# Kernel optimization log

Hardware: AMD Instinct MI355X
Metric: run time of the kernel (lower is better)

Reference implementation:

```python
import jax, jax.numpy as jnp
import numpy as np

CHUNK = 512

def setup_inputs() -> dict:
    key = jax.random.key(0)
    kq, kk, kv = jax.random.split(key, 3)
    shape = (1, 16, 8192, 64)  # B, H, N, E
    return {
        "query": jax.random.normal(kq, shape, dtype=jnp.float32),
        "key": jax.random.normal(kk, shape, dtype=jnp.float32),
        "value": jax.random.normal(kv, shape, dtype=jnp.float32),
    }

def reference(query, key, value):
    c = CHUNK
    B, H, N, E = query.shape
    nc = N // c  # number of query chunks (N assumed divisible by c)
    scale = 1.0 / (E ** 0.5)
    neg_inf = jnp.finfo(query.dtype).min

    qc = query.reshape(B, H, nc, c, E)
    kc = key.reshape(B, H, nc, c, E)
    vc = value.reshape(B, H, nc, c, E)

    # ---- chunk 0: window is just keys[0:c], standard causal mask ----
    s0 = jnp.einsum('bhqe,bhse->bhqs', qc[:, :, 0], kc[:, :, 0]) * scale
    mask0 = jnp.triu(jnp.ones((c, c), dtype=bool), k=1)
    a0 = jax.nn.softmax(jnp.where(mask0, neg_inf, s0), axis=-1)  # (B,H,c,c)
    o0 = jnp.einsum('bhqs,bhse->bhqe', a0, vc[:, :, 0])           # (B,H,c,E)

    # ---- chunks 1..nc-1: key window = [previous chunk, current chunk] ----
    kw = jnp.concatenate([kc[:, :, :-1], kc[:, :, 1:]], axis=3)  # (B,H,nc-1,2c,E)
    vw = jnp.concatenate([vc[:, :, :-1], vc[:, :, 1:]], axis=3)
    s = jnp.einsum('bhnqe,bhnse->bhnqs', qc[:, :, 1:], kw) * scale  # (B,H,nc-1,c,2c)
    # faithful to torch.triu(ones(q_len, k_len), diagonal=1): row r keeps cols 0..r
    mask = jnp.triu(jnp.ones((c, 2 * c), dtype=bool), k=1)
    a = jax.nn.softmax(jnp.where(mask, neg_inf, s), axis=-1)        # (B,H,nc-1,c,2c)
    o = jnp.einsum('bhnqs,bhnse->bhnqe', a, vw)                     # (B,H,nc-1,c,E)

    output = jnp.concatenate([o0, o.reshape(B, H, (nc - 1) * c, E)], axis=2)  # (B,H,N,E)
    # weights concatenated along the key axis (torch cat dim=3)
    a_rest = jnp.moveaxis(a, 2, 3).reshape(B, H, c, (nc - 1) * 2 * c)
    weights = jnp.concatenate([a0, a_rest], axis=3)  # (B,H,c, c + (nc-1)*2c)
    return output, weights
```

## Files before the change

kernel.cpp:

```cpp
#include <hip/hip_runtime.h>

typedef __bf16 bf16x8 __attribute__((ext_vector_type(8)));
typedef float  f32x4  __attribute__((ext_vector_type(4)));

#define NH    16
#define SEQ   8192
#define EDIM  64
#define CHK   512
#define WCOLS 15872
#define OUT0  8388608

#define MFMA(a, b, c) __builtin_amdgcn_mfma_f32_16x16x32_bf16((a), (b), (c), 0, 0, 0)

__global__ __launch_bounds__(512) void chunked_attn_kernel(
    const float* __restrict__ Qg, const float* __restrict__ Kg,
    const float* __restrict__ Vg, float* __restrict__ out)
{
    __shared__ __align__(16) __bf16 lds_k[32768];
    __shared__ __align__(16) __bf16 lds_v[32768];
    __shared__ __align__(16) __bf16 lds_p[8][640];

    const int tid  = threadIdx.x;
    const int lane = tid & 63;
    const int wv   = tid >> 6;
    const int l16  = lane & 15;
    const int quad = lane >> 4;

    const int h  = blockIdx.x >> 4;
    const int n  = blockIdx.x & 15;
    const int ns = (n == 0) ? 0 : n - 1;

    const size_t qbase = ((size_t)h * SEQ + (size_t)n  * CHK) * EDIM;
    const size_t kbase = ((size_t)h * SEQ + (size_t)ns * CHK) * EDIM;
    float* __restrict__ W = out + OUT0;
    const size_t wrow0  = (size_t)h * CHK;
    const int    colbase = (n == 0) ? 0 : (CHK + (n - 1) * 2 * CHK);

    if (n != 0) {
        const size_t z0 = wrow0 * WCOLS + (size_t)(colbase + CHK);
        #pragma unroll 4
        for (int idx = tid; idx < 512 * 128; idx += 512) {
            const int r = idx >> 7, j = idx & 127;
            f32x4 z = {0.f, 0.f, 0.f, 0.f};
            *(f32x4*)(W + z0 + (size_t)r * WCOLS + (size_t)(j * 4)) = z;
        }
    }

    #pragma unroll
    for (int it = 0; it < 8; ++it) {
        const int c = tid + it * 512;
        const int s = c >> 3, sub = c & 7;
        const float* src = Kg + kbase + (size_t)s * EDIM + sub * 8;
        const float4 a = *(const float4*)src;
        const float4 b = *(const float4*)(src + 4);
        bf16x8 t;
        t[0] = (__bf16)a.x; t[1] = (__bf16)a.y; t[2] = (__bf16)a.z; t[3] = (__bf16)a.w;
        t[4] = (__bf16)b.x; t[5] = (__bf16)b.y; t[6] = (__bf16)b.z; t[7] = (__bf16)b.w;
        const int idx = ((s >> 4) * 8 + sub) * 16 + (s & 15);
        ((bf16x8*)lds_k)[idx] = t;
    }

    #pragma unroll
    for (int it = 0; it < 8; ++it) {
        const int c = tid + it * 512;
        const int e = c & 63, sb = c >> 6;
        bf16x8 t;
        #pragma unroll
        for (int j = 0; j < 8; ++j)
            t[j] = (__bf16)Vg[kbase + (size_t)(sb * 8 + j) * EDIM + e];
        const int idx = (((sb >> 2) * 4 + (e >> 4)) * 4 + (sb & 3)) * 16 + (e & 15);
        ((bf16x8*)lds_v)[idx] = t;
    }

    __syncthreads();

    const float SC = 0.125f * 1.44269504088896340736f;
    __bf16* const pb = lds_p[wv];
    const bf16x8* const kf = (const bf16x8*)lds_k;
    const bf16x8* const vf = (const bf16x8*)lds_v;

    for (int mt = 0; mt < 4; ++mt) {
        const int m0 = wv * 64 + mt * 16;
        const int rq = m0 + quad * 4;

        bf16x8 aq0, aq1;
        {
            const float* qp = Qg + qbase + (size_t)(m0 + l16) * EDIM + quad * 8;
            float4 a = *(const float4*)(qp);
            float4 b = *(const float4*)(qp + 4);
            aq0[0]=(__bf16)(a.x*SC); aq0[1]=(__bf16)(a.y*SC); aq0[2]=(__bf16)(a.z*SC); aq0[3]=(__bf16)(a.w*SC);
            aq0[4]=(__bf16)(b.x*SC); aq0[5]=(__bf16)(b.y*SC); aq0[6]=(__bf16)(b.z*SC); aq0[7]=(__bf16)(b.w*SC);
            a = *(const float4*)(qp + 32);
            b = *(const float4*)(qp + 36);
            aq1[0]=(__bf16)(a.x*SC); aq1[1]=(__bf16)(a.y*SC); aq1[2]=(__bf16)(a.z*SC); aq1[3]=(__bf16)(a.w*SC);
            aq1[4]=(__bf16)(b.x*SC); aq1[5]=(__bf16)(b.y*SC); aq1[6]=(__bf16)(b.z*SC); aq1[7]=(__bf16)(b.w*SC);
        }

        float mr[4] = {-3.0e38f, -3.0e38f, -3.0e38f, -3.0e38f};
        float lr[4] = {0.f, 0.f, 0.f, 0.f};
        for (int t = 0; t < 32; ++t) {
            const int kb = t * 128 + quad * 16 + l16;
            f32x4 acc = {0.f, 0.f, 0.f, 0.f};
            acc = MFMA(aq0, kf[kb],      acc);
            acc = MFMA(aq1, kf[kb + 64], acc);
            const int col = t * 16 + l16;
            #pragma unroll
            for (int r = 0; r < 4; ++r) {
                const bool  keep = col <= rq + r;
                const float s  = acc[r];
                const float nm = keep ? fmaxf(mr[r], s) : mr[r];
                lr[r] = lr[r] * __builtin_amdgcn_exp2f(mr[r] - nm)
                      + (keep ? __builtin_amdgcn_exp2f(s - nm) : 0.f);
                mr[r] = nm;
            }
        }

        float ri[4];
        #pragma unroll
        for (int r = 0; r < 4; ++r) {
            #pragma unroll
            for (int off = 1; off < 16; off <<= 1) {
                const float mo = __shfl_xor(mr[r], off);
                const float lo = __shfl_xor(lr[r], off);
                const float nm = fmaxf(mr[r], mo);
                lr[r] = lr[r] * __builtin_amdgcn_exp2f(mr[r] - nm)
                      + lo    * __builtin_amdgcn_exp2f(mo    - nm);
                mr[r] = nm;
            }
            ri[r] = __builtin_amdgcn_rcpf(lr[r]);
        }

        f32x4 o0 = {0,0,0,0}, o1 = {0,0,0,0}, o2 = {0,0,0,0}, o3 = {0,0,0,0};
        const size_t wmt = (wrow0 + (size_t)rq) * WCOLS + colbase;
        for (int pr = 0; pr < 16; ++pr) {
            #pragma unroll
            for (int tt = 0; tt < 2; ++tt) {
                const int t  = pr * 2 + tt;
                const int kb = t * 128 + quad * 16 + l16;
                f32x4 acc = {0.f, 0.f, 0.f, 0.f};
                acc = MFMA(aq0, kf[kb],      acc);
                acc = MFMA(aq1, kf[kb + 64], acc);
                const int col = t * 16 + l16;
                #pragma unroll
                for (int r = 0; r < 4; ++r) {
                    const bool  keep = col <= rq + r;
                    const float p = keep
                        ? __builtin_amdgcn_exp2f(acc[r] - mr[r]) * ri[r] : 0.f;
                    W[wmt + (size_t)r * WCOLS + col] = p;
                    pb[(quad * 4 + r) * 40 + tt * 16 + l16] = (__bf16)p;
                }
            }
            const bf16x8 pa = *(const bf16x8*)(pb + l16 * 40 + quad * 8);
            const int vb = pr * 256 + quad * 16 + l16;
            o0 = MFMA(pa, vf[vb      ], o0);
            o1 = MFMA(pa, vf[vb +  64], o1);
            o2 = MFMA(pa, vf[vb + 128], o2);
            o3 = MFMA(pa, vf[vb + 192], o3);
        }

        const size_t ob = qbase + (size_t)rq * EDIM + l16;
        #pragma unroll
        for (int r = 0; r < 4; ++r) {
            out[ob + (size_t)r * EDIM     ] = o0[r];
            out[ob + (size_t)r * EDIM + 16] = o1[r];
            out[ob + (size_t)r * EDIM + 32] = o2[r];
            out[ob + (size_t)r * EDIM + 48] = o3[r];
        }
    }
}

extern "C" void kernel_launch(void* const* d_in, const int* in_sizes, int n_in,
                              void* d_out, int out_size, void* d_ws, size_t ws_size,
                              hipStream_t stream) {
    const float* Q = (const float*)d_in[0];
    const float* K = (const float*)d_in[1];
    const float* V = (const float*)d_in[2];
    float* out = (float*)d_out;
    chunked_attn_kernel<<<dim3(256), dim3(512), 0, stream>>>(Q, K, V, out);
}
```

Baseline: 648.3 us.

## Cache scores in registers, two-pass softmax, vectorized nontemporal weight stores

Stores the 32 score tiles per row group in registers, so QK^T is computed once and the online softmax becomes an exact max pass followed by an exp-sum pass. The weight matrix is written as vectorized 16-byte nontemporal stores of the bf16-rounded probabilities read back from LDS, replacing scalar strided fp32 stores. Zero-fill and output stores are also nontemporal, and launch bounds ask for two blocks per CU. This trades register pressure (128 floats of scores) and weights now rounded to bf16 precision for fewer MFMAs and better coalesced global writes.

```diff
diff --git a/kernel.cpp b/kernel.cpp
--- a/kernel.cpp
+++ b/kernel.cpp
@@ -12,7 +12,7 @@
 
 #define MFMA(a, b, c) __builtin_amdgcn_mfma_f32_16x16x32_bf16((a), (b), (c), 0, 0, 0)
 
-__global__ __launch_bounds__(512) void chunked_attn_kernel(
+__global__ __launch_bounds__(512, 2) void chunked_attn_kernel(
     const float* __restrict__ Qg, const float* __restrict__ Kg,
     const float* __restrict__ Vg, float* __restrict__ out)
 {
@@ -42,7 +42,7 @@
         for (int idx = tid; idx < 512 * 128; idx += 512) {
             const int r = idx >> 7, j = idx & 127;
             f32x4 z = {0.f, 0.f, 0.f, 0.f};
-            *(f32x4*)(W + z0 + (size_t)r * WCOLS + (size_t)(j * 4)) = z;
+            __builtin_nontemporal_store(z, (f32x4*)(W + z0 + (size_t)r * WCOLS + (size_t)(j * 4)));
         }
     }
 
@@ -96,8 +96,8 @@
             aq1[4]=(__bf16)(b.x*SC); aq1[5]=(__bf16)(b.y*SC); aq1[6]=(__bf16)(b.z*SC); aq1[7]=(__bf16)(b.w*SC);
         }
 
-        float mr[4] = {-3.0e38f, -3.0e38f, -3.0e38f, -3.0e38f};
-        float lr[4] = {0.f, 0.f, 0.f, 0.f};
+        f32x4 st[32];
+        #pragma unroll
         for (int t = 0; t < 32; ++t) {
             const int kb = t * 128 + quad * 16 + l16;
             f32x4 acc = {0.f, 0.f, 0.f, 0.f};
@@ -105,52 +105,67 @@
             acc = MFMA(aq1, kf[kb + 64], acc);
             const int col = t * 16 + l16;
             #pragma unroll
+            for (int r = 0; r < 4; ++r)
+                acc[r] = (col <= rq + r) ? acc[r] : -3.0e38f;
+            st[t] = acc;
+        }
+
+        float mr[4];
+        #pragma unroll
+        for (int r = 0; r < 4; ++r) mr[r] = st[0][r];
+        #pragma unroll
+        for (int t = 1; t < 32; ++t) {
+            #pragma unroll
+            for (int r = 0; r < 4; ++r) mr[r] = fmaxf(mr[r], st[t][r]);
+        }
+        #pragma unroll
+        for (int r = 0; r < 4; ++r) {
+            #pragma unroll
+            for (int off = 1; off < 16; off <<= 1)
+                mr[r] = fmaxf(mr[r], __shfl_xor(mr[r], off));
+        }
+
+        float lr[4] = {0.f, 0.f, 0.f, 0.f};
+        #pragma unroll
+        for (int t = 0; t < 32; ++t) {
+            #pragma unroll
             for (int r = 0; r < 4; ++r) {
-                const bool  keep = col <= rq + r;
-                const float s  = acc[r];
-                const float nm = keep ? fmaxf(mr[r], s) : mr[r];
-                lr[r] = lr[r] * __builtin_amdgcn_exp2f(mr[r] - nm)
-                      + (keep ? __builtin_amdgcn_exp2f(s - nm) : 0.f);
-                mr[r] = nm;
+                const float e = __builtin_amdgcn_exp2f(st[t][r] - mr[r]);
+                st[t][r] = e;
+                lr[r] += e;
             }
         }
-
         float ri[4];
         #pragma unroll
         for (int r = 0; r < 4; ++r) {
             #pragma unroll
-            for (int off = 1; off < 16; off <<= 1) {
-                const float mo = __shfl_xor(mr[r], off);
-                const float lo = __shfl_xor(lr[r], off);
-                const float nm = fmaxf(mr[r], mo);
-                lr[r] = lr[r] * __builtin_amdgcn_exp2f(mr[r] - nm)
-                      + lo    * __builtin_amdgcn_exp2f(mo    - nm);
-                mr[r] = nm;
-            }
+            for (int off = 1; off < 16; off <<= 1)
+                lr[r] += __shfl_xor(lr[r], off);
             ri[r] = __builtin_amdgcn_rcpf(lr[r]);
         }
 
         f32x4 o0 = {0,0,0,0}, o1 = {0,0,0,0}, o2 = {0,0,0,0}, o3 = {0,0,0,0};
-        const size_t wmt = (wrow0 + (size_t)rq) * WCOLS + colbase;
+        float* const wbase = W + (wrow0 + (size_t)(m0 + l16)) * WCOLS + colbase;
+        #pragma unroll
         for (int pr = 0; pr < 16; ++pr) {
             #pragma unroll
             for (int tt = 0; tt < 2; ++tt) {
-                const int t  = pr * 2 + tt;
-                const int kb = t * 128 + quad * 16 + l16;
-                f32x4 acc = {0.f, 0.f, 0.f, 0.f};
-                acc = MFMA(aq0, kf[kb],      acc);
-                acc = MFMA(aq1, kf[kb + 64], acc);
-                const int col = t * 16 + l16;
+                const int t = pr * 2 + tt;
                 #pragma unroll
                 for (int r = 0; r < 4; ++r) {
-                    const bool  keep = col <= rq + r;
-                    const float p = keep
-                        ? __builtin_amdgcn_exp2f(acc[r] - mr[r]) * ri[r] : 0.f;
-                    W[wmt + (size_t)r * WCOLS + col] = p;
+                    const float p = st[t][r] * ri[r];
                     pb[(quad * 4 + r) * 40 + tt * 16 + l16] = (__bf16)p;
                 }
             }
             const bf16x8 pa = *(const bf16x8*)(pb + l16 * 40 + quad * 8);
+            {
+                f32x4 w0, w1;
+                w0[0]=(float)pa[0]; w0[1]=(float)pa[1]; w0[2]=(float)pa[2]; w0[3]=(float)pa[3];
+                w1[0]=(float)pa[4]; w1[1]=(float)pa[5]; w1[2]=(float)pa[6]; w1[3]=(float)pa[7];
+                float* wp = wbase + pr * 32 + quad * 8;
+                __builtin_nontemporal_store(w0, (f32x4*)wp);
+                __builtin_nontemporal_store(w1, (f32x4*)(wp + 4));
+            }
             const int vb = pr * 256 + quad * 16 + l16;
             o0 = MFMA(pa, vf[vb      ], o0);
             o1 = MFMA(pa, vf[vb +  64], o1);
@@ -161,10 +176,10 @@
         const size_t ob = qbase + (size_t)rq * EDIM + l16;
         #pragma unroll
         for (int r = 0; r < 4; ++r) {
-            out[ob + (size_t)r * EDIM     ] = o0[r];
-            out[ob + (size_t)r * EDIM + 16] = o1[r];
-            out[ob + (size_t)r * EDIM + 32] = o2[r];
-            out[ob + (size_t)r * EDIM + 48] = o3[r];
+            __builtin_nontemporal_store(o0[r], out + ob + (size_t)r * EDIM     );
+            __builtin_nontemporal_store(o1[r], out + ob + (size_t)r * EDIM + 16);
+            __builtin_nontemporal_store(o2[r], out + ob + (size_t)r * EDIM + 32);
+            __builtin_nontemporal_store(o3[r], out + ob + (size_t)r * EDIM + 48);
         }
     }
 }
```

After: 657.1 us. No clear change (+1.4%).
